# Performance work log

Hardware: AMD Instinct MI355X
Metric: run time of the kernel (lower is better)

The kernel has to match this reference:

```python
import jax, jax.numpy as jnp
import numpy as np

N_NODES = 100000

def gcn_conv(x, edge_index, W, b):
    # PyG GCNConv: y = D^{-1/2} (A + I) D^{-1/2} X W + b
    N = x.shape[0]
    xw = x @ W  # transform first (smaller feature dim for message passing)
    loop = jnp.arange(N, dtype=edge_index.dtype)
    src = jnp.concatenate([edge_index[0], loop])
    dst = jnp.concatenate([edge_index[1], loop])
    ones = jnp.ones(dst.shape[0], dtype=xw.dtype)
    deg = jax.ops.segment_sum(ones, dst, num_segments=N)
    dinv = jnp.where(deg > 0, jax.lax.rsqrt(deg), 0.0)
    norm = dinv[src] * dinv[dst]  # [E+N]
    msg = xw[src] * norm[:, None]  # gather + scale
    out = jax.ops.segment_sum(msg, dst, num_segments=N)  # scatter-add
    return out + b

def setup_inputs() -> dict:
    key = jax.random.key(0)
    k1, k2, k3, k4, k5 = jax.random.split(key, 5)
    num_features, hidden, num_classes = 500, 64, 40
    x = jax.random.normal(k1, (N_NODES, num_features), dtype=jnp.float32)
    edge_index = jax.random.randint(k2, (2, 1600000), 0, N_NODES, dtype=jnp.int64)
    # Glorot-style init for GCNConv weights, zero bias (PyG default)
    W1 = jax.random.normal(k3, (num_features, hidden), dtype=jnp.float32) / np.sqrt(num_features)
    b1 = jnp.zeros((hidden,), dtype=jnp.float32)
    W2 = jax.random.normal(k4, (hidden, num_classes), dtype=jnp.float32) / np.sqrt(hidden)
    b2 = jnp.zeros((num_classes,), dtype=jnp.float32)
    return {"x": x, "edge_index": edge_index, "W1": W1, "b1": b1, "W2": W2, "b2": b2}

def reference(x, edge_index, W1, b1, W2, b2):
    h = gcn_conv(x, edge_index, W1, b1)
    h = jax.nn.relu(h)
    # dropout is identity in eval mode (training=False)
    logits = gcn_conv(h, edge_index, W2, b2)
    return (jax.nn.log_softmax(logits, axis=1), logits)
```

## Files before the change

kernel.cpp:

```cpp
#include <hip/hip_runtime.h>
#include <hip/hip_bf16.h>
#include <math.h>

#define N_NODES 100000
#define F_IN    500
#define HID     64
#define NCLS    40
#define NBKT    ((N_NODES + 255) / 256)
#define CAP     8192
#define FILL_BLKS 512
#define PREP_ELEMS (HID * 512 + NCLS * HID)
#define PREP_BLKS ((PREP_ELEMS + 255) / 256)
#define GEMM_BLKS ((N_NODES + 127) / 128)

typedef __attribute__((ext_vector_type(8))) short short8v;
typedef __attribute__((ext_vector_type(4))) float floatx4;
typedef unsigned short ushort_t;
typedef unsigned int uint_t;

__device__ __forceinline__ float bflo(uint_t u) {
    union { uint_t i; float f; } v; v.i = u << 16; return v.f;
}
__device__ __forceinline__ float bfhi(uint_t u) {
    union { uint_t i; float f; } v; v.i = u & 0xffff0000u; return v.f;
}
__device__ __forceinline__ ushort_t f2bf(float f) {
    __hip_bfloat16 b = __float2bfloat16(f);
    return *(ushort_t*)&b;
}
__device__ __forceinline__ uint_t pack2(float a, float b) {
    return (uint_t)f2bf(a) | ((uint_t)f2bf(b) << 16);
}

__global__ __launch_bounds__(256) void k1_fill_prep(const int* __restrict__ src,
                                                    const int* __restrict__ dst,
                                                    int* __restrict__ bcount,
                                                    int* __restrict__ pairs,
                                                    const float* __restrict__ W1,
                                                    ushort_t* __restrict__ W1T,
                                                    const float* __restrict__ W2,
                                                    ushort_t* __restrict__ W2bt, int E) {
    if (blockIdx.x >= FILL_BLKS) {
        int idx = (blockIdx.x - FILL_BLKS) * 256 + threadIdx.x;
        if (idx < HID * 512) {
            int nn = idx >> 9;
            int k  = idx & 511;
            float v = (k < F_IN) ? W1[(size_t)k * HID + nn] : 0.0f;
            W1T[idx] = f2bf(v);
        } else if (idx < PREP_ELEMS) {
            int idx2 = idx - HID * 512;
            int nc = idx2 >> 6;
            int k  = idx2 & 63;
            W2bt[idx2] = f2bf(W2[(size_t)k * NCLS + nc]);
        }
        return;
    }
    __shared__ int c[NBKT];
    __shared__ int base[NBKT];
    for (int i = threadIdx.x; i < NBKT; i += 256) c[i] = 0;
    __syncthreads();
    int chunk = (E + FILL_BLKS - 1) / FILL_BLKS;
    int lo = blockIdx.x * chunk;
    int hi = min(lo + chunk, E);
    for (int e = lo + threadIdx.x; e < hi; e += 256) atomicAdd(&c[dst[e] >> 8], 1);
    __syncthreads();
    for (int i = threadIdx.x; i < NBKT; i += 256) {
        int nn = c[i];
        base[i] = nn ? (i * CAP + atomicAdd(&bcount[i], nn)) : 0;
    }
    __syncthreads();
    for (int i = threadIdx.x; i < NBKT; i += 256) c[i] = 0;
    __syncthreads();
    for (int e = lo + threadIdx.x; e < hi; e += 256) {
        int d = dst[e];
        int b = d >> 8;
        int p = base[b] + atomicAdd(&c[b], 1);
        if (p < (b + 1) * CAP) pairs[p] = src[e] | ((d & 255) << 17);
    }
}

__global__ __launch_bounds__(256) void b_fine_kernel(const int* __restrict__ pairs,
                                                     const int* __restrict__ bcount,
                                                     int2* __restrict__ rse,
                                                     int* __restrict__ col,
                                                     float* __restrict__ dinv, int n) {
    __shared__ int w[CAP];
    __shared__ int cnt[256];
    __shared__ int scn[256];
    __shared__ int cur[256];
    int b = blockIdx.x;
    int nb0 = b << 8;
    int nodes = min(256, n - nb0);
    int g0 = b * CAP;
    int size = min(bcount[b], CAP);
    int tid = threadIdx.x;

    for (int i = tid; i < size; i += 256) w[i] = pairs[g0 + i];
    cnt[tid] = 0;
    __syncthreads();
    for (int i = tid; i < size; i += 256) atomicAdd(&cnt[w[i] >> 17], 1);
    __syncthreads();
    int v = cnt[tid];
    scn[tid] = v;
    __syncthreads();
    for (int off = 1; off < 256; off <<= 1) {
        int t = (tid >= off) ? scn[tid - off] : 0;
        __syncthreads();
        scn[tid] += t;
        __syncthreads();
    }
    int excl = scn[tid] - v;
    cur[tid] = g0 + excl;
    if (tid < nodes) {
        rse[nb0 + tid] = make_int2(g0 + excl, g0 + excl + v);
        dinv[nb0 + tid] = rsqrtf((float)(v + 1));
    }
    __syncthreads();
    for (int i = tid; i < size; i += 256) {
        int word = w[i];
        int pos = atomicAdd(&cur[word >> 17], 1);
        col[pos] = word & 0x1FFFF;
    }
}

__global__ __launch_bounds__(256) void gemm1_mfma(const float* __restrict__ x,
                                                  const ushort_t* __restrict__ W1T,
                                                  const float* __restrict__ dinv,
                                                  ushort_t* __restrict__ xws, int n) {
    __shared__ __align__(16) ushort_t As[2][128 * 72];
    const int tid  = threadIdx.x;
    const int wave = tid >> 6;
    const int lane = tid & 63;
    const int m16  = lane & 15;
    const int q    = lane >> 4;
    const int r0   = blockIdx.x * 128;

    floatx4 acc[2][4];
#pragma unroll
    for (int i = 0; i < 2; i++)
#pragma unroll
        for (int j = 0; j < 4; j++) acc[i][j] = (floatx4){0.f, 0.f, 0.f, 0.f};

    const int kg    = tid & 15;
    const int rbase = tid >> 4;

    floatx4 pf[8];
    const floatx4 zero4 = (floatx4){0.f, 0.f, 0.f, 0.f};
    {
        const int k4 = kg * 4;
#pragma unroll
        for (int rr = 0; rr < 8; rr++) {
            int gr = r0 + rbase + rr * 16;
            pf[rr] = (gr < n) ? __builtin_nontemporal_load((const floatx4*)&x[(size_t)gr * F_IN + k4])
                              : zero4;
        }
#pragma unroll
        for (int rr = 0; rr < 8; rr++) {
            int row = rbase + rr * 16;
            *(uint2*)&As[0][row * 72 + kg * 4] =
                make_uint2(pack2(pf[rr][0], pf[rr][1]), pack2(pf[rr][2], pf[rr][3]));
        }
    }
    __syncthreads();

    for (int it = 0; it < 8; it++) {
        const int cur = it & 1;
        if (it < 7) {
            const int k4 = (it + 1) * 64 + kg * 4;
            const bool kok = (k4 < F_IN);
#pragma unroll
            for (int rr = 0; rr < 8; rr++) {
                int gr = r0 + rbase + rr * 16;
                pf[rr] = (kok && gr < n)
                           ? __builtin_nontemporal_load((const floatx4*)&x[(size_t)gr * F_IN + k4])
                           : zero4;
            }
        }
        const int kb = it * 64;
#pragma unroll
        for (int kt = 0; kt < 2; kt++) {
            const int ko = kt * 32 + q * 8;
            short8v a0 = *(const short8v*)&As[cur][(wave * 32 + m16) * 72 + ko];
            short8v a1 = *(const short8v*)&As[cur][(wave * 32 + 16 + m16) * 72 + ko];
#pragma unroll
            for (int nt = 0; nt < 4; nt++) {
                short8v b = *(const short8v*)&W1T[(size_t)(nt * 16 + m16) * 512 + kb + ko];
                acc[0][nt] = __builtin_amdgcn_mfma_f32_16x16x32_bf16(a0, b, acc[0][nt], 0, 0, 0);
                acc[1][nt] = __builtin_amdgcn_mfma_f32_16x16x32_bf16(a1, b, acc[1][nt], 0, 0, 0);
            }
        }
        if (it < 7) {
#pragma unroll
            for (int rr = 0; rr < 8; rr++) {
                int row = rbase + rr * 16;
                *(uint2*)&As[1 - cur][row * 72 + kg * 4] =
                    make_uint2(pack2(pf[rr][0], pf[rr][1]), pack2(pf[rr][2], pf[rr][3]));
            }
            __syncthreads();
        }
    }

#pragma unroll
    for (int mt = 0; mt < 2; mt++) {
#pragma unroll
        for (int i = 0; i < 4; i++) {
            int gr = r0 + wave * 32 + mt * 16 + q * 4 + i;
            if (gr < n) {
                float di = dinv[gr];
#pragma unroll
                for (int nt = 0; nt < 4; nt++) {
                    xws[(size_t)gr * HID + nt * 16 + m16] = f2bf(acc[mt][nt][i] * di);
                }
            }
        }
    }
}

__global__ __launch_bounds__(256) void agg1_kernel(const ushort_t* __restrict__ xws,
                                                   const int* __restrict__ col,
                                                   const int2* __restrict__ rse,
                                                   const float* __restrict__ dinv,
                                                   const float* __restrict__ b1,
                                                   ushort_t* __restrict__ hs, int n) {
    int d = blockIdx.x * 4 + (threadIdx.x >> 6);
    if (d >= n) return;
    int lane = threadIdx.x & 63;
    int g = lane >> 3;
    int c = lane & 7;
    int2 se = rse[d];
    int start = se.x, end = se.y;
    uint4 selfv = *(const uint4*)&xws[(size_t)d * HID + c * 8];
    float acc[8];
#pragma unroll
    for (int i = 0; i < 8; i++) acc[i] = 0.f;
    for (int j = start; j < end; j += 32) {
#pragma unroll
        for (int t = 0; t < 4; t++) {
            int e = j + t * 8 + g;
            if (e < end) {
                int s = col[e];
                uint4 v = *(const uint4*)&xws[(size_t)s * HID + c * 8];
                acc[0] += bflo(v.x); acc[1] += bfhi(v.x);
                acc[2] += bflo(v.y); acc[3] += bfhi(v.y);
                acc[4] += bflo(v.z); acc[5] += bfhi(v.z);
                acc[6] += bflo(v.w); acc[7] += bfhi(v.w);
            }
        }
    }
#pragma unroll
    for (int off = 8; off <= 32; off <<= 1) {
#pragma unroll
        for (int i = 0; i < 8; i++) acc[i] += __shfl_xor(acc[i], off);
    }
    if (g == 0) {
        float di = dinv[d];
        acc[0] += bflo(selfv.x); acc[1] += bfhi(selfv.x);
        acc[2] += bflo(selfv.y); acc[3] += bfhi(selfv.y);
        acc[4] += bflo(selfv.z); acc[5] += bfhi(selfv.z);
        acc[6] += bflo(selfv.w); acc[7] += bfhi(selfv.w);
        float4 b0 = *(const float4*)&b1[c * 8];
        float4 b4 = *(const float4*)&b1[c * 8 + 4];
        uint4 o;
        o.x = pack2(fmaxf(di * acc[0] + b0.x, 0.f) * di, fmaxf(di * acc[1] + b0.y, 0.f) * di);
        o.y = pack2(fmaxf(di * acc[2] + b0.z, 0.f) * di, fmaxf(di * acc[3] + b0.w, 0.f) * di);
        o.z = pack2(fmaxf(di * acc[4] + b4.x, 0.f) * di, fmaxf(di * acc[5] + b4.y, 0.f) * di);
        o.w = pack2(fmaxf(di * acc[6] + b4.z, 0.f) * di, fmaxf(di * acc[7] + b4.w, 0.f) * di);
        *(uint4*)&hs[(size_t)d * HID + c * 8] = o;
    }
}

__global__ __launch_bounds__(256) void gemm2_mfma(const ushort_t* __restrict__ hs,
                                                  const ushort_t* __restrict__ W2bt,
                                                  ushort_t* __restrict__ zs, int n) {
    int wave = threadIdx.x >> 6, lane = threadIdx.x & 63;
    int m16 = lane & 15, q = lane >> 4;
    int r0 = (blockIdx.x * 4 + wave) * 16;
    if (r0 >= n) return;
    floatx4 acc[3];
#pragma unroll
    for (int nt = 0; nt < 3; nt++) acc[nt] = (floatx4){0.f, 0.f, 0.f, 0.f};
#pragma unroll
    for (int kt = 0; kt < 2; kt++) {
        short8v a = *(const short8v*)&hs[(size_t)(r0 + m16) * HID + kt * 32 + q * 8];
#pragma unroll
        for (int nt = 0; nt < 3; nt++) {
            int nc = nt * 16 + m16;
            short8v b;
            if (nc < NCLS) b = *(const short8v*)&W2bt[(size_t)nc * HID + kt * 32 + q * 8];
            else b = (short8v){0, 0, 0, 0, 0, 0, 0, 0};
            acc[nt] = __builtin_amdgcn_mfma_f32_16x16x32_bf16(a, b, acc[nt], 0, 0, 0);
        }
    }
#pragma unroll
    for (int i = 0; i < 4; i++) {
        int gr = r0 + q * 4 + i;
#pragma unroll
        for (int nt = 0; nt < 3; nt++) {
            int cc = nt * 16 + m16;
            if (cc < NCLS) zs[(size_t)gr * NCLS + cc] = f2bf(acc[nt][i]);
        }
    }
}

__global__ __launch_bounds__(256) void agg2_lsm_kernel(const ushort_t* __restrict__ zs,
                                                       const int* __restrict__ col,
                                                       const int2* __restrict__ rse,
                                                       const float* __restrict__ dinv,
                                                       const float* __restrict__ b2,
                                                       float* __restrict__ out, int n) {
    int d = blockIdx.x * 4 + (threadIdx.x >> 6);
    if (d >= n) return;
    int lane = threadIdx.x & 63;
    int g = lane >> 3;
    int c = lane & 7;
    int2 se = rse[d];
    int start = se.x, end = se.y;
    bool act = (c < 5);
    uint4 selfv = make_uint4(0, 0, 0, 0);
    if (act) selfv = *(const uint4*)&zs[(size_t)d * NCLS + c * 8];
    float acc[8];
#pragma unroll
    for (int i = 0; i < 8; i++) acc[i] = 0.f;
    for (int j = start; j < end; j += 32) {
#pragma unroll
        for (int t = 0; t < 4; t++) {
            int e = j + t * 8 + g;
            if (e < end && act) {
                int s = col[e];
                uint4 v = *(const uint4*)&zs[(size_t)s * NCLS + c * 8];
                acc[0] += bflo(v.x); acc[1] += bfhi(v.x);
                acc[2] += bflo(v.y); acc[3] += bfhi(v.y);
                acc[4] += bflo(v.z); acc[5] += bfhi(v.z);
                acc[6] += bflo(v.w); acc[7] += bfhi(v.w);
            }
        }
    }
#pragma unroll
    for (int off = 8; off <= 32; off <<= 1) {
#pragma unroll
        for (int i = 0; i < 8; i++) acc[i] += __shfl_xor(acc[i], off);
    }
    acc[0] += bflo(selfv.x); acc[1] += bfhi(selfv.x);
    acc[2] += bflo(selfv.y); acc[3] += bfhi(selfv.y);
    acc[4] += bflo(selfv.z); acc[5] += bfhi(selfv.z);
    acc[6] += bflo(selfv.w); acc[7] += bfhi(selfv.w);

    float di = dinv[d];
    float4 b0 = make_float4(0.f, 0.f, 0.f, 0.f);
    float4 b4 = make_float4(0.f, 0.f, 0.f, 0.f);
    if (act) {
        b0 = *(const float4*)&b2[c * 8];
        b4 = *(const float4*)&b2[c * 8 + 4];
    }
    float v[8];
    v[0] = di * acc[0] + b0.x; v[1] = di * acc[1] + b0.y;
    v[2] = di * acc[2] + b0.z; v[3] = di * acc[3] + b0.w;
    v[4] = di * acc[4] + b4.x; v[5] = di * acc[5] + b4.y;
    v[6] = di * acc[6] + b4.z; v[7] = di * acc[7] + b4.w;

    float m8 = -INFINITY;
    if (act) {
        m8 = fmaxf(fmaxf(fmaxf(v[0], v[1]), fmaxf(v[2], v[3])),
                   fmaxf(fmaxf(v[4], v[5]), fmaxf(v[6], v[7])));
    }
#pragma unroll
    for (int off = 1; off < 8; off <<= 1) m8 = fmaxf(m8, __shfl_xor(m8, off));
    float s8 = 0.f;
    if (act) {
        s8 = __expf(v[0] - m8) + __expf(v[1] - m8) + __expf(v[2] - m8) + __expf(v[3] - m8)
           + __expf(v[4] - m8) + __expf(v[5] - m8) + __expf(v[6] - m8) + __expf(v[7] - m8);
    }
#pragma unroll
    for (int off = 1; off < 8; off <<= 1) s8 += __shfl_xor(s8, off);

    if (act && g == 0) {
        float lg = __logf(s8);
        float* lsm    = out;
        float* logits = out + (size_t)N_NODES * NCLS;
        float4 lo = make_float4(v[0], v[1], v[2], v[3]);
        float4 hi = make_float4(v[4], v[5], v[6], v[7]);
        *(float4*)&logits[(size_t)d * NCLS + c * 8]     = lo;
        *(float4*)&logits[(size_t)d * NCLS + c * 8 + 4] = hi;
        float4 olo, ohi;
        olo.x = v[0] - m8 - lg; olo.y = v[1] - m8 - lg;
        olo.z = v[2] - m8 - lg; olo.w = v[3] - m8 - lg;
        ohi.x = v[4] - m8 - lg; ohi.y = v[5] - m8 - lg;
        ohi.z = v[6] - m8 - lg; ohi.w = v[7] - m8 - lg;
        *(float4*)&lsm[(size_t)d * NCLS + c * 8]     = olo;
        *(float4*)&lsm[(size_t)d * NCLS + c * 8 + 4] = ohi;
    }
}

extern "C" void kernel_launch(void* const* d_in, const int* in_sizes, int n_in,
                              void* d_out, int out_size, void* d_ws, size_t ws_size,
                              hipStream_t stream) {
    const float* x  = (const float*)d_in[0];
    const int*   ei = (const int*)d_in[1];
    const float* W1 = (const float*)d_in[2];
    const float* b1 = (const float*)d_in[3];
    const float* W2 = (const float*)d_in[4];
    const float* b2 = (const float*)d_in[5];

    const int N = N_NODES;
    const int E = in_sizes[1] / 2;
    const int* src = ei;
    const int* dst = ei + E;

    ushort_t* xws  = (ushort_t*)d_ws;
    ushort_t* hsb  = xws + (size_t)N * HID;
    ushort_t* zsb  = hsb + (size_t)N * HID;
    ushort_t* W1T  = zsb + (size_t)N * NCLS;
    ushort_t* W2bt = W1T + (size_t)HID * 512;
    float* dinv    = (float*)(W2bt + NCLS * HID);
    int2*  rse     = (int2*)(dinv + N);
    int*   bcount  = (int*)(rse + N);
    int*   pairs   = bcount + 512;
    int*   col     = pairs + (size_t)NBKT * CAP;

    const int NB_W = (N + 3) / 4;

    (void)hipMemsetAsync(bcount, 0, 512 * sizeof(int), stream);

    k1_fill_prep<<<FILL_BLKS + PREP_BLKS, 256, 0, stream>>>(src, dst, bcount, pairs,
                                                           W1, W1T, W2, W2bt, E);

    b_fine_kernel<<<NBKT, 256, 0, stream>>>(pairs, bcount, rse, col, dinv, N);

    gemm1_mfma<<<GEMM_BLKS, 256, 0, stream>>>(x, W1T, dinv, xws, N);

    agg1_kernel<<<NB_W, 256, 0, stream>>>(xws, col, rse, dinv, b1, hsb, N);

    gemm2_mfma<<<(N / 16 + 3) / 4, 256, 0, stream>>>(hsb, W2bt, zsb, N);

    agg2_lsm_kernel<<<NB_W, 256, 0, stream>>>(zsb, col, rse, dinv, b2, (float*)d_out, N);
}
```

Measured before the change: 475.8 us.

## Assign eight lanes per node in aggregation kernels instead of a full wave

Both aggregation kernels now map each destination node to an 8-lane group, so one wave handles 8 nodes instead of 1. Each group walks that node's edges serially with a 4-way unrolled gather and no cross-group shuffle reduction. With an average degree of about 17, the old one-wave-per-node layout left most of its 8 edge groups idle and paid a shuffle reduction per node. The tradeoffs are fewer gathers in flight per node, and divergence when nodes in the same wave have very different degrees.

```diff
diff --git a/kernel.cpp b/kernel.cpp
--- a/kernel.cpp
+++ b/kernel.cpp
@@ -222,51 +222,49 @@
                                                    const float* __restrict__ dinv,
                                                    const float* __restrict__ b1,
                                                    ushort_t* __restrict__ hs, int n) {
-    int d = blockIdx.x * 4 + (threadIdx.x >> 6);
+    int d = blockIdx.x * 32 + (threadIdx.x >> 3);
     if (d >= n) return;
-    int lane = threadIdx.x & 63;
-    int g = lane >> 3;
-    int c = lane & 7;
+    int c = threadIdx.x & 7;
     int2 se = rse[d];
-    int start = se.x, end = se.y;
-    uint4 selfv = *(const uint4*)&xws[(size_t)d * HID + c * 8];
     float acc[8];
-#pragma unroll
-    for (int i = 0; i < 8; i++) acc[i] = 0.f;
-    for (int j = start; j < end; j += 32) {
-#pragma unroll
-        for (int t = 0; t < 4; t++) {
-            int e = j + t * 8 + g;
-            if (e < end) {
-                int s = col[e];
-                uint4 v = *(const uint4*)&xws[(size_t)s * HID + c * 8];
-                acc[0] += bflo(v.x); acc[1] += bfhi(v.x);
-                acc[2] += bflo(v.y); acc[3] += bfhi(v.y);
-                acc[4] += bflo(v.z); acc[5] += bfhi(v.z);
-                acc[6] += bflo(v.w); acc[7] += bfhi(v.w);
-            }
-        }
-    }
-#pragma unroll
-    for (int off = 8; off <= 32; off <<= 1) {
-#pragma unroll
-        for (int i = 0; i < 8; i++) acc[i] += __shfl_xor(acc[i], off);
-    }
-    if (g == 0) {
-        float di = dinv[d];
-        acc[0] += bflo(selfv.x); acc[1] += bfhi(selfv.x);
-        acc[2] += bflo(selfv.y); acc[3] += bfhi(selfv.y);
-        acc[4] += bflo(selfv.z); acc[5] += bfhi(selfv.z);
-        acc[6] += bflo(selfv.w); acc[7] += bfhi(selfv.w);
-        float4 b0 = *(const float4*)&b1[c * 8];
-        float4 b4 = *(const float4*)&b1[c * 8 + 4];
-        uint4 o;
-        o.x = pack2(fmaxf(di * acc[0] + b0.x, 0.f) * di, fmaxf(di * acc[1] + b0.y, 0.f) * di);
-        o.y = pack2(fmaxf(di * acc[2] + b0.z, 0.f) * di, fmaxf(di * acc[3] + b0.w, 0.f) * di);
-        o.z = pack2(fmaxf(di * acc[4] + b4.x, 0.f) * di, fmaxf(di * acc[5] + b4.y, 0.f) * di);
-        o.w = pack2(fmaxf(di * acc[6] + b4.z, 0.f) * di, fmaxf(di * acc[7] + b4.w, 0.f) * di);
-        *(uint4*)&hs[(size_t)d * HID + c * 8] = o;
-    }
+    uint4 sv = *(const uint4*)&xws[(size_t)d * HID + c * 8];
+    acc[0] = bflo(sv.x); acc[1] = bfhi(sv.x);
+    acc[2] = bflo(sv.y); acc[3] = bfhi(sv.y);
+    acc[4] = bflo(sv.z); acc[5] = bfhi(sv.z);
+    acc[6] = bflo(sv.w); acc[7] = bfhi(sv.w);
+    int e = se.x;
+    for (; e + 4 <= se.y; e += 4) {
+        int s0 = col[e], s1 = col[e + 1], s2 = col[e + 2], s3 = col[e + 3];
+        uint4 v0 = *(const uint4*)&xws[(size_t)s0 * HID + c * 8];
+        uint4 v1 = *(const uint4*)&xws[(size_t)s1 * HID + c * 8];
+        uint4 v2 = *(const uint4*)&xws[(size_t)s2 * HID + c * 8];
+        uint4 v3 = *(const uint4*)&xws[(size_t)s3 * HID + c * 8];
+        acc[0] += bflo(v0.x) + bflo(v1.x) + bflo(v2.x) + bflo(v3.x);
+        acc[1] += bfhi(v0.x) + bfhi(v1.x) + bfhi(v2.x) + bfhi(v3.x);
+        acc[2] += bflo(v0.y) + bflo(v1.y) + bflo(v2.y) + bflo(v3.y);
+        acc[3] += bfhi(v0.y) + bfhi(v1.y) + bfhi(v2.y) + bfhi(v3.y);
+        acc[4] += bflo(v0.z) + bflo(v1.z) + bflo(v2.z) + bflo(v3.z);
+        acc[5] += bfhi(v0.z) + bfhi(v1.z) + bfhi(v2.z) + bfhi(v3.z);
+        acc[6] += bflo(v0.w) + bflo(v1.w) + bflo(v2.w) + bflo(v3.w);
+        acc[7] += bfhi(v0.w) + bfhi(v1.w) + bfhi(v2.w) + bfhi(v3.w);
+    }
+    for (; e < se.y; e++) {
+        int s = col[e];
+        uint4 v = *(const uint4*)&xws[(size_t)s * HID + c * 8];
+        acc[0] += bflo(v.x); acc[1] += bfhi(v.x);
+        acc[2] += bflo(v.y); acc[3] += bfhi(v.y);
+        acc[4] += bflo(v.z); acc[5] += bfhi(v.z);
+        acc[6] += bflo(v.w); acc[7] += bfhi(v.w);
+    }
+    float di = dinv[d];
+    float4 b0 = *(const float4*)&b1[c * 8];
+    float4 b4 = *(const float4*)&b1[c * 8 + 4];
+    uint4 o;
+    o.x = pack2(fmaxf(di * acc[0] + b0.x, 0.f) * di, fmaxf(di * acc[1] + b0.y, 0.f) * di);
+    o.y = pack2(fmaxf(di * acc[2] + b0.z, 0.f) * di, fmaxf(di * acc[3] + b0.w, 0.f) * di);
+    o.z = pack2(fmaxf(di * acc[4] + b4.x, 0.f) * di, fmaxf(di * acc[5] + b4.y, 0.f) * di);
+    o.w = pack2(fmaxf(di * acc[6] + b4.z, 0.f) * di, fmaxf(di * acc[7] + b4.w, 0.f) * di);
+    *(uint4*)&hs[(size_t)d * HID + c * 8] = o;
 }
 
 __global__ __launch_bounds__(256) void gemm2_mfma(const ushort_t* __restrict__ hs,
@@ -308,42 +306,45 @@
                                                        const float* __restrict__ dinv,
                                                        const float* __restrict__ b2,
                                                        float* __restrict__ out, int n) {
-    int d = blockIdx.x * 4 + (threadIdx.x >> 6);
+    int d = blockIdx.x * 32 + (threadIdx.x >> 3);
     if (d >= n) return;
-    int lane = threadIdx.x & 63;
-    int g = lane >> 3;
-    int c = lane & 7;
+    int c = threadIdx.x & 7;
+    bool act = (c < 5);
     int2 se = rse[d];
-    int start = se.x, end = se.y;
-    bool act = (c < 5);
-    uint4 selfv = make_uint4(0, 0, 0, 0);
-    if (act) selfv = *(const uint4*)&zs[(size_t)d * NCLS + c * 8];
     float acc[8];
 #pragma unroll
     for (int i = 0; i < 8; i++) acc[i] = 0.f;
-    for (int j = start; j < end; j += 32) {
-#pragma unroll
-        for (int t = 0; t < 4; t++) {
-            int e = j + t * 8 + g;
-            if (e < end && act) {
-                int s = col[e];
-                uint4 v = *(const uint4*)&zs[(size_t)s * NCLS + c * 8];
-                acc[0] += bflo(v.x); acc[1] += bfhi(v.x);
-                acc[2] += bflo(v.y); acc[3] += bfhi(v.y);
-                acc[4] += bflo(v.z); acc[5] += bfhi(v.z);
-                acc[6] += bflo(v.w); acc[7] += bfhi(v.w);
-            }
-        }
-    }
-#pragma unroll
-    for (int off = 8; off <= 32; off <<= 1) {
-#pragma unroll
-        for (int i = 0; i < 8; i++) acc[i] += __shfl_xor(acc[i], off);
-    }
-    acc[0] += bflo(selfv.x); acc[1] += bfhi(selfv.x);
-    acc[2] += bflo(selfv.y); acc[3] += bfhi(selfv.y);
-    acc[4] += bflo(selfv.z); acc[5] += bfhi(selfv.z);
-    acc[6] += bflo(selfv.w); acc[7] += bfhi(selfv.w);
+    if (act) {
+        uint4 sv = *(const uint4*)&zs[(size_t)d * NCLS + c * 8];
+        acc[0] = bflo(sv.x); acc[1] = bfhi(sv.x);
+        acc[2] = bflo(sv.y); acc[3] = bfhi(sv.y);
+        acc[4] = bflo(sv.z); acc[5] = bfhi(sv.z);
+        acc[6] = bflo(sv.w); acc[7] = bfhi(sv.w);
+        int e = se.x;
+        for (; e + 4 <= se.y; e += 4) {
+            int s0 = col[e], s1 = col[e + 1], s2 = col[e + 2], s3 = col[e + 3];
+            uint4 v0 = *(const uint4*)&zs[(size_t)s0 * NCLS + c * 8];
+            uint4 v1 = *(const uint4*)&zs[(size_t)s1 * NCLS + c * 8];
+            uint4 v2 = *(const uint4*)&zs[(size_t)s2 * NCLS + c * 8];
+            uint4 v3 = *(const uint4*)&zs[(size_t)s3 * NCLS + c * 8];
+            acc[0] += bflo(v0.x) + bflo(v1.x) + bflo(v2.x) + bflo(v3.x);
+            acc[1] += bfhi(v0.x) + bfhi(v1.x) + bfhi(v2.x) + bfhi(v3.x);
+            acc[2] += bflo(v0.y) + bflo(v1.y) + bflo(v2.y) + bflo(v3.y);
+            acc[3] += bfhi(v0.y) + bfhi(v1.y) + bfhi(v2.y) + bfhi(v3.y);
+            acc[4] += bflo(v0.z) + bflo(v1.z) + bflo(v2.z) + bflo(v3.z);
+            acc[5] += bfhi(v0.z) + bfhi(v1.z) + bfhi(v2.z) + bfhi(v3.z);
+            acc[6] += bflo(v0.w) + bflo(v1.w) + bflo(v2.w) + bflo(v3.w);
+            acc[7] += bfhi(v0.w) + bfhi(v1.w) + bfhi(v2.w) + bfhi(v3.w);
+        }
+        for (; e < se.y; e++) {
+            int s = col[e];
+            uint4 v = *(const uint4*)&zs[(size_t)s * NCLS + c * 8];
+            acc[0] += bflo(v.x); acc[1] += bfhi(v.x);
+            acc[2] += bflo(v.y); acc[3] += bfhi(v.y);
+            acc[4] += bflo(v.z); acc[5] += bfhi(v.z);
+            acc[6] += bflo(v.w); acc[7] += bfhi(v.w);
+        }
+    }
 
     float di = dinv[d];
     float4 b0 = make_float4(0.f, 0.f, 0.f, 0.f);
@@ -373,7 +374,7 @@
 #pragma unroll
     for (int off = 1; off < 8; off <<= 1) s8 += __shfl_xor(s8, off);
 
-    if (act && g == 0) {
+    if (act) {
         float lg = __logf(s8);
         float* lsm    = out;
         float* logits = out + (size_t)N_NODES * NCLS;
@@ -417,7 +418,7 @@
     int*   pairs   = bcount + 512;
     int*   col     = pairs + (size_t)NBKT * CAP;
 
-    const int NB_W = (N + 3) / 4;
+    const int NB_A = (N + 31) / 32;
 
     (void)hipMemsetAsync(bcount, 0, 512 * sizeof(int), stream);
 
@@ -428,9 +429,9 @@
 
     gemm1_mfma<<<GEMM_BLKS, 256, 0, stream>>>(x, W1T, dinv, xws, N);
 
-    agg1_kernel<<<NB_W, 256, 0, stream>>>(xws, col, rse, dinv, b1, hsb, N);
+    agg1_kernel<<<NB_A, 256, 0, stream>>>(xws, col, rse, dinv, b1, hsb, N);
 
     gemm2_mfma<<<(N / 16 + 3) / 4, 256, 0, stream>>>(hsb, W2bt, zsb, N);
 
-    agg2_lsm_kernel<<<NB_W, 256, 0, stream>>>(zsb, col, rse, dinv, b2, (float*)d_out, N);
-}
+    agg2_lsm_kernel<<<NB_A, 256, 0, stream>>>(zsb, col, rse, dinv, b2, (float*)d_out, N);
+}
```

Result: faster. 441.4 us (-7.2%).
